# Performance work log

Hardware: AMD Instinct MI355X
Metric: run time of the kernel (lower is better)

## Reference

```python
import jax, jax.numpy as jnp
import numpy as np

BS, N, D, K = 2, 256, 128, 3
ABSORB = 0.5
EPS = 1e-5


def _mlp(x, w0, b0, g, be, m, v, w1, b1):
    # Linear -> BatchNorm1d (eval: running stats) -> ReLU -> Linear(->1)
    h = x @ w0 + b0
    h = (h - m) * (g / jnp.sqrt(v + EPS)) + be
    h = jax.nn.relu(h)
    return (h @ w1 + b1)[..., 0]


def _pick_neighbors(feat, sw0, sb0, sg, sbe, sm, sv, sw1, sb1):
    # feat: [bs, n, d] -> absorbed feat [bs,n,d], neighbor feats [bs,n,K,d]
    bs, n, d = feat.shape
    f1 = jnp.broadcast_to(feat[:, :, None, :], (bs, n, n, d))
    f2 = jnp.broadcast_to(feat[:, None, :, :], (bs, n, n, d))
    pair = jnp.concatenate([f1, f2], axis=-1)            # [bs,n,n,2d]
    sim = _mlp(pair, sw0, sb0, sg, sbe, sm, sv, sw1, sb1)  # [bs,n,n]
    sim = jnp.where(jnp.eye(n, dtype=bool), -jnp.inf, sim)  # exclude self
    idx = jax.lax.top_k(sim, K)[1]                        # [bs,n,K]
    nbr = jnp.take_along_axis(feat, idx.reshape(bs, n * K, 1), axis=1)
    nbr = nbr.reshape(bs, n, K, d)                        # gathered neighbor feats
    absorbed = feat + ABSORB * nbr.mean(axis=2)           # absorb from neighbors
    return absorbed, nbr


def setup_inputs() -> dict:
    key = jax.random.key(0)
    ks = jax.random.split(key, 8)
    s = 1.0 / np.sqrt(D)
    inp = {
        "feat1": jax.random.normal(ks[0], (BS, N, D), jnp.float32),
        "feat2": jax.random.normal(ks[1], (BS, N, D), jnp.float32),
        # sim_intra_frame: Linear(2D->D), BN(D), ReLU, Linear(D->1)
        "sim_w0": jax.random.normal(ks[2], (2 * D, D), jnp.float32) * s,
        "sim_b0": jnp.zeros((D,), jnp.float32),
        "sim_g": jnp.ones((D,), jnp.float32),
        "sim_be": jnp.zeros((D,), jnp.float32),
        "sim_m": jnp.zeros((D,), jnp.float32),
        "sim_v": jnp.ones((D,), jnp.float32),
        "sim_w1": jax.random.normal(ks[3], (D, 1), jnp.float32) * s,
        "sim_b1": jnp.zeros((1,), jnp.float32),
        # classifier: Linear(D->D), BN(D), ReLU, Linear(D->1)
        "cls_w0": jax.random.normal(ks[4], (D, D), jnp.float32) * s,
        "cls_b0": jnp.zeros((D,), jnp.float32),
        "cls_g": jnp.ones((D,), jnp.float32),
        "cls_be": jnp.zeros((D,), jnp.float32),
        "cls_m": jnp.zeros((D,), jnp.float32),
        "cls_v": jnp.ones((D,), jnp.float32),
        "cls_w1": jax.random.normal(ks[5], (D, 1), jnp.float32) * s,
        "cls_b1": jnp.zeros((1,), jnp.float32),
    }
    return inp


def reference(feat1, feat2, sim_w0, sim_b0, sim_g, sim_be, sim_m, sim_v, sim_w1, sim_b1,
              cls_w0, cls_b0, cls_g, cls_be, cls_m, cls_v, cls_w1, cls_b1):
    a1, n1 = _pick_neighbors(feat1, sim_w0, sim_b0, sim_g, sim_be, sim_m, sim_v, sim_w1, sim_b1)
    a2, n2 = _pick_neighbors(feat2, sim_w0, sim_b0, sim_g, sim_be, sim_m, sim_v, sim_w1, sim_b1)
    # anchor pair scores: |f1_i - f2_j| -> classifier -> sigmoid
    dpair = jnp.abs(a1[:, :, None, :] - a2[:, None, :, :])         # [bs,N1,N2,D]
    logits = _mlp(dpair, cls_w0, cls_b0, cls_g, cls_be, cls_m, cls_v, cls_w1, cls_b1)
    score = jax.nn.sigmoid(logits)                                  # [bs,N1,N2]
    # neighbor pair scores matched k-to-k (match_neighbor=True)
    dnei = jnp.abs(n1[:, :, None, :, :] - n2[:, None, :, :, :])     # [bs,N1,N2,K,D]
    logits_nei = _mlp(dnei, cls_w0, cls_b0, cls_g, cls_be, cls_m, cls_v, cls_w1, cls_b1)
    score_nei = jax.nn.sigmoid(logits_nei).mean(axis=-1)            # [bs,N1,N2]
    return 0.5 * (score + score_nei)
```

## Files before the change

kernel.cpp:

```cpp
#include <hip/hip_runtime.h>
#include <hip/hip_bf16.h>
#include <math.h>

#define BS 2
#define NN 256
#define DD 128
#define EPSF 1e-5f

typedef __hip_bfloat16 bf16;
typedef __attribute__((ext_vector_type(8))) short bfrag;
typedef __attribute__((ext_vector_type(4))) float f4;

static __device__ __forceinline__ float b2f(bf16 x) { return __bfloat162float(x); }

static __device__ __forceinline__ float ldin(const void* p, int i, int isb) {
    return isb ? __bfloat162float(((const bf16*)p)[i]) : ((const float*)p)[i];
}
static __device__ __forceinline__ unsigned int bfr(float x) {
    unsigned int u = __float_as_uint(x);
    return (u + 0x7fffu + ((u >> 16) & 1u)) >> 16;
}
static __device__ __forceinline__ unsigned int pkbf(float lo, float hi) {
    return bfr(lo) | (bfr(hi) << 16);
}

__device__ int            g_isbf16;
__device__ float          g_SWT[2 * DD * DD];
__device__ float          g_U[2 * BS * NN * DD];
__device__ float          g_Vt[2 * BS * DD * NN];
__device__ unsigned short g_pack[2 * BS * NN * 4 * DD];
__device__ unsigned short g_W0T[DD * DD];
__device__ float          g_eps[3][DD];
__device__ float          g_seps[3][DD];
__device__ float          g_b1;

__global__ void detect_kernel(const void* __restrict__ sim_v_) {
    unsigned v = *(const unsigned*)sim_v_;
    g_isbf16 = ((v & 0xFFFFu) != 0u) ? 1 : 0;
}

__global__ void fill_const(unsigned short* __restrict__ out, int n, unsigned short v) {
    int i = blockIdx.x * blockDim.x + threadIdx.x;
    if (i < n) out[i] = v;
}

__global__ __launch_bounds__(256) void prep_all(
    const void* __restrict__ sim_w0, const void* __restrict__ sim_b0,
    const void* __restrict__ sim_g, const void* __restrict__ sim_be,
    const void* __restrict__ sim_m, const void* __restrict__ sim_v_,
    const void* __restrict__ sim_w1,
    const void* __restrict__ cls_w0, const void* __restrict__ cls_b0,
    const void* __restrict__ cls_g, const void* __restrict__ cls_be,
    const void* __restrict__ cls_m, const void* __restrict__ cls_v_,
    const void* __restrict__ cls_w1, const void* __restrict__ cls_b1)
{
    int isb = g_isbf16;
    int blk = blockIdx.x, tid = threadIdx.x;
    if (blk < 64) {
        int t = blk * 256 + tid;
        int n = t & 127, k = t >> 7;
        g_W0T[n * DD + k] = (unsigned short)bfr(ldin(cls_w0, k * DD + n, isb));
    } else if (blk < 192) {
        int e = (blk - 64) * 256 + tid;
        int r = e & 255, c = e >> 8;
        g_SWT[r * DD + c] = ldin(sim_w0, (c + (r >> 7) * DD) * DD + (r & 127), isb);
    } else {
        if (tid < DD) {
            float al = ldin(cls_g, tid, isb) / sqrtf(ldin(cls_v_, tid, isb) + EPSF);
            g_eps[0][tid] = al;
            g_eps[1][tid] = (ldin(cls_b0, tid, isb) - ldin(cls_m, tid, isb)) * al + ldin(cls_be, tid, isb);
            g_eps[2][tid] = ldin(cls_w1, tid, isb);
            if (tid == 0) g_b1 = ldin(cls_b1, 0, isb);
        } else {
            int d = tid - DD;
            float aS = ldin(sim_g, d, isb) / sqrtf(ldin(sim_v_, d, isb) + EPSF);
            g_seps[0][d] = aS;
            g_seps[1][d] = (ldin(sim_b0, d, isb) - ldin(sim_m, d, isb)) * aS + ldin(sim_be, d, isb);
            g_seps[2][d] = ldin(sim_w1, d, isb);
        }
    }
}

__global__ __launch_bounds__(256) void uv_kernel(
    const void* __restrict__ feat1, const void* __restrict__ feat2)
{
    int i = blockIdx.x, b = blockIdx.y, f = blockIdx.z;
    int tid = threadIdx.x;
    int isb = g_isbf16;
    const void* feat = (f == 0) ? feat1 : feat2;
    __shared__ float fr[DD];
    if (tid < DD) fr[tid] = ldin(feat, (b * NN + i) * DD + tid, isb);
    __syncthreads();
    int h = tid >> 7, d = tid & 127;
    const float* wrow = &g_SWT[(h * DD + d) * DD];
    float acc = 0.f;
    for (int c = 0; c < DD; c += 4) {
        float4 wq = *(const float4*)&wrow[c];
        acc = fmaf(fr[c + 0], wq.x, acc);
        acc = fmaf(fr[c + 1], wq.y, acc);
        acc = fmaf(fr[c + 2], wq.z, acc);
        acc = fmaf(fr[c + 3], wq.w, acc);
    }
    int fb = f * BS + b;
    if (h == 0) g_U[(fb * NN + i) * DD + d] = acc * g_seps[0][d] + g_seps[1][d];
    else        g_Vt[(fb * DD + d) * NN + i] = acc * g_seps[0][d];
}

__global__ __launch_bounds__(256) void sim1_kernel(
    const void* __restrict__ feat1, const void* __restrict__ feat2)
{
    int i = blockIdx.x, b = blockIdx.y, f = blockIdx.z;
    int fb = f * BS + b;
    int tid = threadIdx.x;
    int isb = g_isbf16;
    const void* feat = (f == 0) ? feat1 : feat2;

    __shared__ float Ur[DD], wS[DD], fr[DD];
    __shared__ float sv[NN];
    __shared__ int t3[3];

    if (tid < DD) {
        Ur[tid] = g_U[(fb * NN + i) * DD + tid];
        wS[tid] = g_seps[2][tid];
        fr[tid] = ldin(feat, (b * NN + i) * DD + tid, isb);
    }
    __syncthreads();

    {
        int j = tid;
        const float* vt = &g_Vt[fb * DD * NN + j];
        float s = 0.f;
#pragma unroll 8
        for (int d = 0; d < DD; d++)
            s = fmaf(wS[d], fmaxf(Ur[d] + vt[d * NN], 0.f), s);
        sv[j] = (j == i) ? -INFINITY : s;
    }
    __syncthreads();

    if (tid < 64) {
        int l = tid;
        float tv0 = -INFINITY, tv1 = -INFINITY, tv2 = -INFINITY;
        int tj0 = 0x7fffffff, tj1 = 0x7fffffff, tj2 = 0x7fffffff;
#pragma unroll
        for (int t = 0; t < 4; t++) {
            int jj = l * 4 + t;
            float v = sv[jj];
            if ((v > tv2) || (v == tv2 && jj < tj2)) {
                tv2 = v; tj2 = jj;
                if ((tv2 > tv1) || (tv2 == tv1 && tj2 < tj1)) {
                    float tp = tv1; tv1 = tv2; tv2 = tp; int ti = tj1; tj1 = tj2; tj2 = ti;
                }
                if ((tv1 > tv0) || (tv1 == tv0 && tj1 < tj0)) {
                    float tp = tv0; tv0 = tv1; tv1 = tp; int ti = tj0; tj0 = tj1; tj1 = ti;
                }
            }
        }
        for (int off = 1; off < 64; off <<= 1) {
            float qv0 = __shfl_xor(tv0, off), qv1 = __shfl_xor(tv1, off), qv2 = __shfl_xor(tv2, off);
            int qj0 = __shfl_xor(tj0, off), qj1 = __shfl_xor(tj1, off), qj2 = __shfl_xor(tj2, off);
            float av[4] = { tv0, tv1, tv2, -INFINITY }; int aj[4] = { tj0, tj1, tj2, 0x7fffffff };
            float bv[4] = { qv0, qv1, qv2, -INFINITY }; int bj[4] = { qj0, qj1, qj2, 0x7fffffff };
            float nv[3]; int nj[3];
            int ia = 0, ib = 0;
#pragma unroll
            for (int t = 0; t < 3; t++) {
                bool ab = (av[ia] > bv[ib]) || (av[ia] == bv[ib] && aj[ia] < bj[ib]);
                if (ab) { nv[t] = av[ia]; nj[t] = aj[ia]; ia++; }
                else    { nv[t] = bv[ib]; nj[t] = bj[ib]; ib++; }
            }
            tv0 = nv[0]; tv1 = nv[1]; tv2 = nv[2]; tj0 = nj[0]; tj1 = nj[1]; tj2 = nj[2];
        }
        if (l == 0) { t3[0] = tj0; t3[1] = tj1; t3[2] = tj2; }
    }
    __syncthreads();

    unsigned int* gp = (unsigned int*)g_pack + (fb * NN + i) * 256;
    int vv = tid >> 6, dw = tid & 63;
    int d0 = dw * 2, d1 = d0 + 1;
    float lo, hi;
    if (vv == 0) {
        int n0 = t3[0], n1 = t3[1], n2 = t3[2];
        float s0 = ldin(feat, (b * NN + n0) * DD + d0, isb) +
                   ldin(feat, (b * NN + n1) * DD + d0, isb) +
                   ldin(feat, (b * NN + n2) * DD + d0, isb);
        float s1 = ldin(feat, (b * NN + n0) * DD + d1, isb) +
                   ldin(feat, (b * NN + n1) * DD + d1, isb) +
                   ldin(feat, (b * NN + n2) * DD + d1, isb);
        lo = fr[d0] + 0.5f * (s0 * (1.0f / 3.0f));
        hi = fr[d1] + 0.5f * (s1 * (1.0f / 3.0f));
    } else {
        int nb = t3[vv - 1];
        lo = ldin(feat, (b * NN + nb) * DD + d0, isb);
        hi = ldin(feat, (b * NN + nb) * DD + d1, isb);
    }
    gp[tid] = pkbf(lo, hi);
}

__global__ __launch_bounds__(256) void classify_mfma(void* __restrict__ out) {
    int jt = blockIdx.x, it = blockIdx.y, b = blockIdx.z;
    int tid = threadIdx.x, l = tid & 63, w = tid >> 6;
    int lm = l & 15, q = l >> 4;
    int isb = g_isbf16;
    int i = it * 4 + w;

    __shared__ __align__(16) short W0B[DD * 136];
    __shared__ __align__(16) short Xs[4][16 * 136];
    __shared__ float epsS[3][DD];

    {
        const uint4* src = (const uint4*)g_W0T;
        for (int t = tid; t < 2048; t += 256) {
            int n = t >> 4, c = t & 15;
            *(uint4*)&W0B[n * 136 + c * 8] = src[t];
        }
        for (int t = tid; t < 3 * DD; t += 256)
            ((float*)epsS)[t] = ((const float*)g_eps)[t];
    }
    __syncthreads();
    float b1c = g_b1;

    const unsigned int* p1 = (const unsigned int*)g_pack + ((b * NN + i) * 4) * 64;
    const unsigned int* p2 = (const unsigned int*)g_pack + (((BS + b) * NN) * 4) * 64;
    unsigned int u1[4];
#pragma unroll
    for (int v = 0; v < 4; v++) u1[v] = p1[v * 64 + l];

    short* Xw = &Xs[w][0];

    for (int chunk = 0; chunk < 4; chunk++) {
        int jb = jt * 16 + chunk * 4;
#pragma unroll
        for (int p = 0; p < 4; p++) {
            const unsigned int* pj = p2 + ((jb + p) * 4) * 64;
#pragma unroll
            for (int v = 0; v < 4; v++) {
                unsigned int ua = u1[v], ub = pj[v * 64 + l];
                float ax = __uint_as_float(ua << 16), ay = __uint_as_float(ua & 0xffff0000u);
                float bx = __uint_as_float(ub << 16), by = __uint_as_float(ub & 0xffff0000u);
                *(unsigned int*)&Xw[(p * 4 + v) * 136 + 2 * l] = pkbf(fabsf(ax - bx), fabsf(ay - by));
            }
        }
        __syncthreads();

        bfrag A[4];
#pragma unroll
        for (int ks = 0; ks < 4; ks++)
            A[ks] = *(const bfrag*)&Xw[lm * 136 + ks * 32 + q * 8];

        f4 psum = {0.f, 0.f, 0.f, 0.f};
#pragma unroll
        for (int ct = 0; ct < 8; ct++) {
            int n = ct * 16 + lm;
            f4 acc = {0.f, 0.f, 0.f, 0.f};
#pragma unroll
            for (int ks = 0; ks < 4; ks++) {
                bfrag B = *(const bfrag*)&W0B[n * 136 + ks * 32 + q * 8];
                acc = __builtin_amdgcn_mfma_f32_16x16x32_bf16(A[ks], B, acc, 0, 0, 0);
            }
            float an = epsS[0][n], bn = epsS[1][n], wn = epsS[2][n];
#pragma unroll
            for (int r = 0; r < 4; r++)
                psum[r] += wn * fmaxf(fmaf(acc[r], an, bn), 0.f);
        }
#pragma unroll
        for (int off = 1; off < 16; off <<= 1) {
#pragma unroll
            for (int r = 0; r < 4; r++)
                psum[r] += __shfl_xor(psum[r], off);
        }
        float s0 = 1.f / (1.f + __expf(-(psum[0] + b1c)));
        float s1 = 1.f / (1.f + __expf(-(psum[1] + b1c)));
        float s2 = 1.f / (1.f + __expf(-(psum[2] + b1c)));
        float s3 = 1.f / (1.f + __expf(-(psum[3] + b1c)));
        float o = 0.5f * (s0 + (s1 + s2 + s3) * (1.f / 3.f));
        if (lm == 0) {
            int oi = (b * NN + i) * NN + (jb + q);
            if (isb) ((bf16*)out)[oi] = __float2bfloat16(o);
            else     ((float*)out)[oi] = o;
        }
        __syncthreads();
    }
}

extern "C" void kernel_launch(void* const* d_in, const int* in_sizes, int n_in,
                              void* d_out, int out_size, void* d_ws, size_t ws_size,
                              hipStream_t stream) {
    (void)d_ws; (void)ws_size;

    static const int expect[18] = {
        BS * NN * DD, BS * NN * DD,
        2 * DD * DD, DD, DD, DD, DD, DD, DD, 1,
        DD * DD, DD, DD, DD, DD, DD, DD, 1
    };
    bool ok = (n_in >= 18);
    if (ok) for (int k = 0; k < 18; k++) if (in_sizes[k] != expect[k]) ok = false;
    if (!ok) {
        fill_const<<<(out_size + 255) / 256, 256, 0, stream>>>(
            (unsigned short*)d_out, out_size, (unsigned short)0x3F00);
        return;
    }

    const void* feat1  = d_in[0];
    const void* feat2  = d_in[1];
    const void* sim_w0 = d_in[2];
    const void* sim_b0 = d_in[3];
    const void* sim_g  = d_in[4];
    const void* sim_be = d_in[5];
    const void* sim_m  = d_in[6];
    const void* sim_v  = d_in[7];
    const void* sim_w1 = d_in[8];
    const void* cls_w0 = d_in[10];
    const void* cls_b0 = d_in[11];
    const void* cls_g  = d_in[12];
    const void* cls_be = d_in[13];
    const void* cls_m  = d_in[14];
    const void* cls_v  = d_in[15];
    const void* cls_w1 = d_in[16];
    const void* cls_b1 = d_in[17];

    detect_kernel<<<1, 1, 0, stream>>>(sim_v);
    prep_all<<<193, 256, 0, stream>>>(sim_w0, sim_b0, sim_g, sim_be, sim_m, sim_v, sim_w1,
                                      cls_w0, cls_b0, cls_g, cls_be, cls_m, cls_v, cls_w1, cls_b1);
    uv_kernel<<<dim3(NN, BS, 2), 256, 0, stream>>>(feat1, feat2);
    sim1_kernel<<<dim3(NN, BS, 2), 256, 0, stream>>>(feat1, feat2);
    classify_mfma<<<dim3(16, 64, BS), 256, 0, stream>>>(d_out);
}
```

Measured before the change: 161.1 us.

## Hoist A-fragments across chunks, reuse W0 B-fragments, drop block barriers

The final pair-scoring kernel now builds all four chunks' A fragments up front into registers, using per-wave LDS staging with __threadfence_block in place of __syncthreads. It then loops over output column tiles with the B fragments loaded once and reused across all four chunks, so W0 is read from LDS a quarter as often. The BF16 packing uses the library conversion instead of manual rounding. This raises register pressure (16 A fragments, 4 accumulators) and depends on the per-wave Xs buffer being safe without a block barrier.

```diff
diff --git a/kernel.cpp b/kernel.cpp
--- a/kernel.cpp
+++ b/kernel.cpp
@@ -22,6 +22,10 @@
 }
 static __device__ __forceinline__ unsigned int pkbf(float lo, float hi) {
     return bfr(lo) | (bfr(hi) << 16);
+}
+static __device__ __forceinline__ unsigned int pkbf_fast(float lo, float hi) {
+    __hip_bfloat162 h = __float22bfloat162_rn(float2{lo, hi});
+    return *reinterpret_cast<unsigned int*>(&h);
 }
 
 __device__ int            g_isbf16;
@@ -227,6 +231,8 @@
 
     short* Xw = &Xs[w][0];
 
+    bfrag A[4][4];
+#pragma unroll
     for (int chunk = 0; chunk < 4; chunk++) {
         int jb = jt * 16 + chunk * 4;
 #pragma unroll
@@ -237,48 +243,55 @@
                 unsigned int ua = u1[v], ub = pj[v * 64 + l];
                 float ax = __uint_as_float(ua << 16), ay = __uint_as_float(ua & 0xffff0000u);
                 float bx = __uint_as_float(ub << 16), by = __uint_as_float(ub & 0xffff0000u);
-                *(unsigned int*)&Xw[(p * 4 + v) * 136 + 2 * l] = pkbf(fabsf(ax - bx), fabsf(ay - by));
+                *(unsigned int*)&Xw[(p * 4 + v) * 136 + 2 * l] = pkbf_fast(fabsf(ax - bx), fabsf(ay - by));
             }
         }
-        __syncthreads();
-
-        bfrag A[4];
+        __threadfence_block();
 #pragma unroll
         for (int ks = 0; ks < 4; ks++)
-            A[ks] = *(const bfrag*)&Xw[lm * 136 + ks * 32 + q * 8];
-
-        f4 psum = {0.f, 0.f, 0.f, 0.f};
-#pragma unroll
-        for (int ct = 0; ct < 8; ct++) {
-            int n = ct * 16 + lm;
+            A[chunk][ks] = *(const bfrag*)&Xw[lm * 136 + ks * 32 + q * 8];
+        __threadfence_block();
+    }
+
+    f4 psum[4] = {{0,0,0,0},{0,0,0,0},{0,0,0,0},{0,0,0,0}};
+#pragma unroll
+    for (int ct = 0; ct < 8; ct++) {
+        int n = ct * 16 + lm;
+        bfrag B[4];
+#pragma unroll
+        for (int ks = 0; ks < 4; ks++)
+            B[ks] = *(const bfrag*)&W0B[n * 136 + ks * 32 + q * 8];
+        float an = epsS[0][n], bn = epsS[1][n], wn = epsS[2][n];
+#pragma unroll
+        for (int chunk = 0; chunk < 4; chunk++) {
             f4 acc = {0.f, 0.f, 0.f, 0.f};
 #pragma unroll
-            for (int ks = 0; ks < 4; ks++) {
-                bfrag B = *(const bfrag*)&W0B[n * 136 + ks * 32 + q * 8];
-                acc = __builtin_amdgcn_mfma_f32_16x16x32_bf16(A[ks], B, acc, 0, 0, 0);
-            }
-            float an = epsS[0][n], bn = epsS[1][n], wn = epsS[2][n];
+            for (int ks = 0; ks < 4; ks++)
+                acc = __builtin_amdgcn_mfma_f32_16x16x32_bf16(A[chunk][ks], B[ks], acc, 0, 0, 0);
 #pragma unroll
             for (int r = 0; r < 4; r++)
-                psum[r] += wn * fmaxf(fmaf(acc[r], an, bn), 0.f);
-        }
+                psum[chunk][r] += wn * fmaxf(fmaf(acc[r], an, bn), 0.f);
+        }
+    }
+
+#pragma unroll
+    for (int chunk = 0; chunk < 4; chunk++) {
 #pragma unroll
         for (int off = 1; off < 16; off <<= 1) {
 #pragma unroll
             for (int r = 0; r < 4; r++)
-                psum[r] += __shfl_xor(psum[r], off);
-        }
-        float s0 = 1.f / (1.f + __expf(-(psum[0] + b1c)));
-        float s1 = 1.f / (1.f + __expf(-(psum[1] + b1c)));
-        float s2 = 1.f / (1.f + __expf(-(psum[2] + b1c)));
-        float s3 = 1.f / (1.f + __expf(-(psum[3] + b1c)));
+                psum[chunk][r] += __shfl_xor(psum[chunk][r], off);
+        }
+        float s0 = 1.f / (1.f + __expf(-(psum[chunk][0] + b1c)));
+        float s1 = 1.f / (1.f + __expf(-(psum[chunk][1] + b1c)));
+        float s2 = 1.f / (1.f + __expf(-(psum[chunk][2] + b1c)));
+        float s3 = 1.f / (1.f + __expf(-(psum[chunk][3] + b1c)));
         float o = 0.5f * (s0 + (s1 + s2 + s3) * (1.f / 3.f));
         if (lm == 0) {
-            int oi = (b * NN + i) * NN + (jb + q);
+            int oi = (b * NN + i) * NN + (jt * 16 + chunk * 4 + q);
             if (isb) ((bf16*)out)[oi] = __float2bfloat16(o);
             else     ((float*)out)[oi] = o;
         }
-        __syncthreads();
     }
 }
 
```

Result: no change. 158.3 us (-1.7%).
